# Optimization experiments

Hardware: AMD Instinct MI355X
Metric: run time of the kernel (lower is better)

The kernel has to match this reference:

```python
import jax, jax.numpy as jnp
import numpy as np

D_EMB = 1024
D_ATTN = 1024
NUM_HEADS = 16
HEAD_DIM = D_ATTN // NUM_HEADS
SEQ = 2048
BS = 2


def setup_inputs() -> dict:
    key = jax.random.key(0)
    ks = jax.random.split(key, 6)
    s = 1.0 / np.sqrt(D_EMB)
    return {
        "x": jax.random.normal(ks[0], (BS, SEQ, D_EMB), dtype=jnp.float32),
        "W_q": jax.random.uniform(ks[1], (D_ATTN, D_EMB), jnp.float32, -s, s),
        "W_k": jax.random.uniform(ks[2], (D_ATTN, D_EMB), jnp.float32, -s, s),
        "W_v": jax.random.uniform(ks[3], (D_ATTN, D_EMB), jnp.float32, -s, s),
        "W_o": jax.random.uniform(ks[4], (D_ATTN, D_ATTN), jnp.float32, -s, s),
        "b_o": jax.random.uniform(ks[5], (D_ATTN,), jnp.float32, -s, s),
    }


def reference(x, W_q, W_k, W_v, W_o, b_o):
    bs, seq_len, _ = x.shape
    # QKV projections (torch Linear: x @ W.T)
    q = jnp.einsum('bse,ae->bsa', x, W_q).reshape(bs, seq_len, NUM_HEADS, HEAD_DIM)
    k = jnp.einsum('bse,ae->bsa', x, W_k).reshape(bs, seq_len, NUM_HEADS, HEAD_DIM)
    v = jnp.einsum('bse,ae->bsa', x, W_v).reshape(bs, seq_len, NUM_HEADS, HEAD_DIM)
    # [b, h, s, d]
    q = q.transpose(0, 2, 1, 3)
    k = k.transpose(0, 2, 1, 3)
    v = v.transpose(0, 2, 1, 3)
    # scores [b, h, s, s] with causal mask
    scores = jnp.einsum('bhqd,bhkd->bhqk', q, k)
    causal = jnp.tril(jnp.ones((seq_len, seq_len), dtype=bool))
    scores = jnp.where(causal, scores, -jnp.inf)
    attn = jax.nn.softmax(scores / np.sqrt(HEAD_DIM), axis=-1)
    # dropout p=0.0 -> identity
    ctx = jnp.einsum('bhqk,bhkd->bhqd', attn, v)
    ctx = ctx.transpose(0, 2, 1, 3).reshape(bs, seq_len, D_ATTN)
    return jnp.einsum('bsa,oa->bso', ctx, W_o) + b_o
```

## Files before the change

kernel.cpp:

```cpp
#include <hip/hip_runtime.h>
#include <stdint.h>

#define SEQ   2048
#define DEMB  1024
#define NH    16
#define HD    64
#define MROWS 4096

typedef __bf16 bf16x8 __attribute__((ext_vector_type(8)));
typedef __bf16 bf16x4 __attribute__((ext_vector_type(4)));
typedef float  f32x4  __attribute__((ext_vector_type(4)));

#define MFMA(a, b, c) __builtin_amdgcn_mfma_f32_16x16x32_bf16((a), (b), (c), 0, 0, 0)

static __device__ __forceinline__ uint16_t f2bf(float f) {
  union { __bf16 b; uint16_t u; } c;
  c.b = (__bf16)f;
  return c.u;
}

static __device__ __forceinline__ ushort4 pack4(f32x4 f) {
  union { bf16x4 b; ushort4 u; } c;
  c.b[0] = (__bf16)f[0]; c.b[1] = (__bf16)f[1];
  c.b[2] = (__bf16)f[2]; c.b[3] = (__bf16)f[3];
  return c.u;
}

static __device__ __forceinline__ bf16x8 ldb8(const uint16_t* p) {
  union { uint4 i; bf16x8 b; } u;
  u.i = *(const uint4*)p;
  return u.b;
}

static __device__ __forceinline__ void gld_lds16(const uint16_t* g, uint16_t* l) {
  __builtin_amdgcn_global_load_lds(
      (const __attribute__((address_space(1))) uint32_t*)(g),
      (__attribute__((address_space(3))) uint32_t*)(l),
      16, 0, 0);
}

__global__ __launch_bounds__(256) void cvt_all(const float* __restrict__ x,
                                               const float* __restrict__ wq,
                                               const float* __restrict__ wk,
                                               const float* __restrict__ wv,
                                               const float* __restrict__ wo,
                                               uint16_t* __restrict__ xb,
                                               uint16_t* __restrict__ wqkv,
                                               uint16_t* __restrict__ wob) {
  const int bid = blockIdx.x;
  const float* src; uint16_t* dst; int off;
  if (bid < 4096)      { src = x;  dst = xb;                 off = bid; }
  else if (bid < 5120) { src = wq; dst = wqkv;               off = bid - 4096; }
  else if (bid < 6144) { src = wk; dst = wqkv + (1u << 20);  off = bid - 5120; }
  else if (bid < 7168) { src = wv; dst = wqkv + (2u << 20);  off = bid - 6144; }
  else                 { src = wo; dst = wob;                off = bid - 7168; }
  const int i = (off * 256 + threadIdx.x) * 4;
  float4 v = *(const float4*)(src + i);
  f32x4 f; f[0] = v.x; f[1] = v.y; f[2] = v.z; f[3] = v.w;
  *(ushort4*)(dst + i) = pack4(f);
}

template <int MODE>
__global__ __launch_bounds__(256) void gemm_bt(const uint16_t* __restrict__ A,
                                               const uint16_t* __restrict__ B,
                                               uint16_t* __restrict__ Cq,
                                               uint16_t* __restrict__ Ck,
                                               uint16_t* __restrict__ Cvt,
                                               float* __restrict__ Cf,
                                               const float* __restrict__ bias,
                                               int K) {
  constexpr int BN = (MODE == 2) ? 64 : 128;
  constexpr int NI = (MODE == 2) ? 2 : 4;
  __shared__ uint16_t As[2][128 * 32];
  __shared__ uint16_t Bs[2][BN * 32];
  const int t  = threadIdx.x;
  const int l  = t & 63;
  const int li = l & 15, lg = l >> 4;
  const int w  = t >> 6;
  const int wr = (w >> 1) << 6;
  const int wc = (MODE == 2) ? ((w & 1) << 5) : ((w & 1) << 6);
  const int brow = blockIdx.y << 7;
  const int bcol = blockIdx.x * BN;

  const int st_row = t >> 2;
  const int st_col = ((t & 3) ^ (st_row & 3) ^ ((st_row >> 2) & 3)) * 8;
  const uint16_t* ga0 = A + (size_t)(brow + st_row) * K + st_col;
  const uint16_t* ga1 = ga0 + (size_t)64 * K;
  const uint16_t* gb0 = B + (size_t)(bcol + st_row) * K + st_col;
  const uint16_t* gb1 = gb0 + (size_t)64 * K;

  auto stage = [&](int buf, int k0) {
    gld_lds16(ga0 + k0, &As[buf][t * 8]);
    gld_lds16(ga1 + k0, &As[buf][2048 + t * 8]);
    gld_lds16(gb0 + k0, &Bs[buf][t * 8]);
    if (BN == 128) gld_lds16(gb1 + k0, &Bs[buf][2048 + t * 8]);
  };

  const int rx = (li & 3) ^ (li >> 2);
  const int rcol = (lg ^ rx) * 8;

  f32x4 acc[4][NI] = {};

  stage(0, 0);
  __syncthreads();
  int cur = 0;

  for (int k0 = 0; k0 < K; k0 += 32) {
    if (k0 + 32 < K) stage(cur ^ 1, k0 + 32);

    bf16x8 af[4], bfr[NI];
#pragma unroll
    for (int i = 0; i < 4; ++i)
      af[i] = ldb8(&As[cur][(wr + i * 16 + li) * 32 + rcol]);
#pragma unroll
    for (int i = 0; i < NI; ++i)
      bfr[i] = ldb8(&Bs[cur][(wc + i * 16 + li) * 32 + rcol]);
#pragma unroll
    for (int mi = 0; mi < 4; ++mi)
#pragma unroll
      for (int ni = 0; ni < NI; ++ni)
        acc[mi][ni] = MFMA(af[mi], bfr[ni], acc[mi][ni]);

    __syncthreads();
    cur ^= 1;
  }

#pragma unroll
  for (int mi = 0; mi < 4; ++mi) {
#pragma unroll
    for (int ni = 0; ni < NI; ++ni) {
      const int row = brow + wr + mi * 16 + lg * 4;
      const int col = bcol + wc + ni * 16 + li;
#pragma unroll
      for (int r = 0; r < 4; ++r) {
        const float v = acc[mi][ni][r];
        if (MODE == 0) {
          if (col < 1024) {
            Cq[(size_t)(row + r) * 1024 + col] = f2bf(v * 0.18033688f);
          } else if (col < 2048) {
            Ck[(size_t)(row + r) * 1024 + (col - 1024)] = f2bf(v);
          } else {
            const int c = col - 2048;
            const int m = row + r;
            Cvt[((size_t)c + (size_t)((m >> 11) << 10)) * 2048 + (m & 2047)] = f2bf(v);
          }
        } else {
          Cf[(size_t)(row + r) * 1024 + col] = v + bias[col];
        }
      }
    }
  }
}

__global__ __launch_bounds__(256) void attn_fwd(const uint16_t* __restrict__ Q,
                                                const uint16_t* __restrict__ K,
                                                const uint16_t* __restrict__ Vt,
                                                uint16_t* __restrict__ ctx) {
  const int bh = blockIdx.x;
  const int qb = 31 - blockIdx.y;
  const int b  = bh >> 4, h = bh & 15;
  const int t  = threadIdx.x;
  const int w  = t >> 6, l = t & 63;
  const int li = l & 15, lg = l >> 4;

  __shared__ uint16_t Kl[2][64 * 64];
  __shared__ uint16_t Vl[2][64 * 64];
  __shared__ uint16_t P[4][16][72];

  const uint16_t* Kg = K + (size_t)(b * 2048) * 1024 + h * 64;
  const uint16_t* Vg = Vt + (size_t)(b * 1024 + h * 64) * 2048;

  const int srow = t >> 3;
  const int scol = ((t & 7) * 8) ^ ((srow & 7) * 8);

  const int qrow = (qb << 6) + (w << 4);
  const uint16_t* qp = Q + (size_t)(b * 2048 + qrow + li) * 1024 + h * 64 + lg * 8;
  const bf16x8 q0 = ldb8(qp);
  const bf16x8 q1 = ldb8(qp + 32);

  f32x4 o[4] = {};
  float l_r = 0.f;

  auto stage = [&](int buf, int kt2) {
    const int kb2 = kt2 << 6;
    gld_lds16(Kg + (size_t)(kb2 + srow) * 1024 + scol,      &Kl[buf][t * 8]);
    gld_lds16(Kg + (size_t)(kb2 + 32 + srow) * 1024 + scol, &Kl[buf][2048 + t * 8]);
    gld_lds16(Vg + (size_t)srow * 2048 + kb2 + scol,        &Vl[buf][t * 8]);
    gld_lds16(Vg + (size_t)(32 + srow) * 2048 + kb2 + scol, &Vl[buf][2048 + t * 8]);
  };

  stage(0, 0);
  __syncthreads();
  int cur = 0;

  const int fsw = (li & 7) * 8;

  for (int kt = 0; kt <= qb; ++kt) {
    if (kt < qb) stage(cur ^ 1, kt + 1);

    const uint16_t* Kc = &Kl[cur][0];
    const uint16_t* Vc = &Vl[cur][0];

    f32x4 s[4];
    __builtin_amdgcn_s_setprio(1);
#pragma unroll
    for (int tt = 0; tt < 4; ++tt) {
      const uint16_t* kr = Kc + (tt * 16 + li) * 64;
      f32x4 z = {};
      z = MFMA(ldb8(kr + ((lg * 8) ^ fsw)), q0, z);
      z = MFMA(ldb8(kr + ((32 + lg * 8) ^ fsw)), q1, z);
      s[tt] = z;
    }
    __builtin_amdgcn_s_setprio(0);

    bf16x8 vf[4][2];
#pragma unroll
    for (int dt = 0; dt < 4; ++dt) {
      const uint16_t* vr = Vc + (dt * 16 + li) * 64;
      vf[dt][0] = ldb8(vr + ((lg * 8) ^ fsw));
      vf[dt][1] = ldb8(vr + ((32 + lg * 8) ^ fsw));
    }

    if (kt == qb) {
      const int qloc = (w << 4) + li;
#pragma unroll
      for (int tt = 0; tt < 4; ++tt) {
        const int key = (tt << 4) + (lg << 2);
#pragma unroll
        for (int r = 0; r < 4; ++r)
          if (key + r > qloc) s[tt][r] = -1e30f;
      }
    }

    float lsum = 0.f;
    ushort4 pk[4];
#pragma unroll
    for (int tt = 0; tt < 4; ++tt) {
      f32x4 p;
      p[0] = __builtin_amdgcn_exp2f(s[tt][0]);
      p[1] = __builtin_amdgcn_exp2f(s[tt][1]);
      p[2] = __builtin_amdgcn_exp2f(s[tt][2]);
      p[3] = __builtin_amdgcn_exp2f(s[tt][3]);
      lsum += (p[0] + p[1]) + (p[2] + p[3]);
      pk[tt] = pack4(p);
    }
    l_r += lsum;

#pragma unroll
    for (int tt = 0; tt < 4; ++tt)
      *(ushort4*)&P[w][li][(tt << 4) + (lg << 2)] = pk[tt];
    asm volatile("s_waitcnt lgkmcnt(0)" ::: "memory");

    const bf16x8 pb0 = ldb8(&P[w][li][lg * 8]);
    const bf16x8 pb1 = ldb8(&P[w][li][32 + lg * 8]);
    __builtin_amdgcn_s_setprio(1);
#pragma unroll
    for (int dt = 0; dt < 4; ++dt) {
      o[dt] = MFMA(vf[dt][0], pb0, o[dt]);
      o[dt] = MFMA(vf[dt][1], pb1, o[dt]);
    }
    __builtin_amdgcn_s_setprio(0);

    __syncthreads();
    cur ^= 1;
  }

  l_r += __shfl_xor(l_r, 16);
  l_r += __shfl_xor(l_r, 32);
  const float inv = 1.0f / l_r;
  const int qg = b * 2048 + qrow + li;
#pragma unroll
  for (int dt = 0; dt < 4; ++dt) {
    f32x4 ov = o[dt];
    ov[0] *= inv; ov[1] *= inv; ov[2] *= inv; ov[3] *= inv;
    *(ushort4*)(ctx + (size_t)qg * 1024 + h * 64 + (dt << 4) + (lg << 2)) = pack4(ov);
  }
}

extern "C" void kernel_launch(void* const* d_in, const int* in_sizes, int n_in,
                              void* d_out, int out_size, void* d_ws, size_t ws_size,
                              hipStream_t stream) {
  const float* x  = (const float*)d_in[0];
  const float* Wq = (const float*)d_in[1];
  const float* Wk = (const float*)d_in[2];
  const float* Wv = (const float*)d_in[3];
  const float* Wo = (const float*)d_in[4];
  const float* bo = (const float*)d_in[5];
  float* out = (float*)d_out;

  char* ws = (char*)d_ws;
  uint16_t* xb   = (uint16_t*)(ws);
  uint16_t* Wqkv = (uint16_t*)(ws + ( 8u << 20));
  uint16_t* Wob  = (uint16_t*)(ws + (14u << 20));
  uint16_t* Qb   = (uint16_t*)(ws + (16u << 20));
  uint16_t* Kb   = (uint16_t*)(ws + (24u << 20));
  uint16_t* Vt   = (uint16_t*)(ws + (32u << 20));
  uint16_t* Ctx  = (uint16_t*)(ws);

  cvt_all<<<8192, 256, 0, stream>>>(x, Wq, Wk, Wv, Wo, xb, Wqkv, Wob);

  gemm_bt<0><<<dim3(24, 32), 256, 0, stream>>>(xb, Wqkv, Qb, Kb, Vt,
                                               nullptr, nullptr, 1024);

  attn_fwd<<<dim3(32, 32), 256, 0, stream>>>(Qb, Kb, Vt, Ctx);

  gemm_bt<2><<<dim3(16, 32), 256, 0, stream>>>(Ctx, Wob, nullptr, nullptr, nullptr,
                                               out, bo, 1024);
}
```

Measured before the change: 112.1 us.

## Use 512-thread blocks, K=64 stages, XCD-aware block swizzle for GEMMs and attention

Both GEMMs move to 512-thread blocks with eight waves, a 64-wide K stage with an XOR swizzle for LDS, and a 1D grid remapped so each group of eight consecutive block IDs covers a contiguous chunk of tiles. The aim is better L2 locality per XCD and fewer barriers per K. Attention now handles 128 query rows per block with eight waves sharing each K/V tile, and orders (batch, head) pairs by XCD. This halves K/V staging per query, though each wave now waits on more barriers and causal masking spans two diagonal tiles.

```diff
diff --git a/kernel.cpp b/kernel.cpp
--- a/kernel.cpp
+++ b/kernel.cpp
@@ -61,43 +61,55 @@
 }
 
 template <int MODE>
-__global__ __launch_bounds__(256) void gemm_bt(const uint16_t* __restrict__ A,
+__global__ __launch_bounds__(512) void gemm_bt(const uint16_t* __restrict__ A,
                                                const uint16_t* __restrict__ B,
                                                uint16_t* __restrict__ Cq,
                                                uint16_t* __restrict__ Ck,
                                                uint16_t* __restrict__ Cvt,
                                                float* __restrict__ Cf,
-                                               const float* __restrict__ bias,
-                                               int K) {
-  constexpr int BN = (MODE == 2) ? 64 : 128;
-  constexpr int NI = (MODE == 2) ? 2 : 4;
-  __shared__ uint16_t As[2][128 * 32];
-  __shared__ uint16_t Bs[2][BN * 32];
+                                               const float* __restrict__ bias) {
+  constexpr int K   = 1024;
+  constexpr int BN  = (MODE == 0) ? 128 : 64;
+  constexpr int NI  = (MODE == 0) ? 2 : 1;
+  constexpr int NBX = (MODE == 0) ? 24 : 16;
+  constexpr int CHUNK = (MODE == 0) ? 96 : 64;
+
+  __shared__ uint16_t As[2][128 * 64];
+  __shared__ uint16_t Bs[2][BN * 64];
+
+  const int id  = blockIdx.x;
+  const int swz = (id & 7) * CHUNK + (id >> 3);
+  const int brow = (swz / NBX) << 7;
+  const int bcol = (swz % NBX) * BN;
+
   const int t  = threadIdx.x;
   const int l  = t & 63;
   const int li = l & 15, lg = l >> 4;
   const int w  = t >> 6;
-  const int wr = (w >> 1) << 6;
-  const int wc = (MODE == 2) ? ((w & 1) << 5) : ((w & 1) << 6);
-  const int brow = blockIdx.y << 7;
-  const int bcol = blockIdx.x * BN;
-
-  const int st_row = t >> 2;
-  const int st_col = ((t & 3) ^ (st_row & 3) ^ ((st_row >> 2) & 3)) * 8;
-  const uint16_t* ga0 = A + (size_t)(brow + st_row) * K + st_col;
-  const uint16_t* ga1 = ga0 + (size_t)64 * K;
-  const uint16_t* gb0 = B + (size_t)(bcol + st_row) * K + st_col;
-  const uint16_t* gb1 = gb0 + (size_t)64 * K;
+  const int wm = w >> 2;
+  const int wn = w & 3;
+
+  const int srow = t >> 3;
+  const int scol = ((t & 7) ^ (srow & 7)) << 3;
+  const uint16_t* gA = A + (size_t)(brow + srow) * K + scol;
+  const uint16_t* gB = B + (size_t)(bcol + srow) * K + scol;
 
   auto stage = [&](int buf, int k0) {
-    gld_lds16(ga0 + k0, &As[buf][t * 8]);
-    gld_lds16(ga1 + k0, &As[buf][2048 + t * 8]);
-    gld_lds16(gb0 + k0, &Bs[buf][t * 8]);
-    if (BN == 128) gld_lds16(gb1 + k0, &Bs[buf][2048 + t * 8]);
+    gld_lds16(gA + k0, &As[buf][t * 8]);
+    gld_lds16(gA + (size_t)64 * K + k0, &As[buf][4096 + t * 8]);
+    gld_lds16(gB + k0, &Bs[buf][t * 8]);
+    if (MODE == 0) gld_lds16(gB + (size_t)64 * K + k0, &Bs[buf][4096 + t * 8]);
   };
 
-  const int rx = (li & 3) ^ (li >> 2);
-  const int rcol = (lg ^ rx) * 8;
+  const int sw = li & 7;
+  auto ldA = [&](int buf, int kh, int fi) {
+    const int row = wm * 64 + fi * 16 + li;
+    return ldb8(&As[buf][(row << 6) + ((((kh << 2) + lg) ^ sw) << 3)]);
+  };
+  auto ldB = [&](int buf, int kh, int ni) {
+    const int row = wn * (BN / 4) + ni * 16 + li;
+    return ldb8(&Bs[buf][(row << 6) + ((((kh << 2) + lg) ^ sw) << 3)]);
+  };
 
   f32x4 acc[4][NI] = {};
 
@@ -105,21 +117,24 @@
   __syncthreads();
   int cur = 0;
 
-  for (int k0 = 0; k0 < K; k0 += 32) {
-    if (k0 + 32 < K) stage(cur ^ 1, k0 + 32);
-
-    bf16x8 af[4], bfr[NI];
-#pragma unroll
-    for (int i = 0; i < 4; ++i)
-      af[i] = ldb8(&As[cur][(wr + i * 16 + li) * 32 + rcol]);
-#pragma unroll
-    for (int i = 0; i < NI; ++i)
-      bfr[i] = ldb8(&Bs[cur][(wc + i * 16 + li) * 32 + rcol]);
-#pragma unroll
-    for (int mi = 0; mi < 4; ++mi)
-#pragma unroll
-      for (int ni = 0; ni < NI; ++ni)
-        acc[mi][ni] = MFMA(af[mi], bfr[ni], acc[mi][ni]);
+  for (int k0 = 0; k0 < K; k0 += 64) {
+    if (k0 + 64 < K) stage(cur ^ 1, k0 + 64);
+
+#pragma unroll
+    for (int kh = 0; kh < 2; ++kh) {
+      bf16x8 af[4], bfr[NI];
+#pragma unroll
+      for (int fi = 0; fi < 4; ++fi) af[fi] = ldA(cur, kh, fi);
+#pragma unroll
+      for (int ni = 0; ni < NI; ++ni) bfr[ni] = ldB(cur, kh, ni);
+      __builtin_amdgcn_s_setprio(1);
+#pragma unroll
+      for (int fi = 0; fi < 4; ++fi)
+#pragma unroll
+        for (int ni = 0; ni < NI; ++ni)
+          acc[fi][ni] = MFMA(af[fi], bfr[ni], acc[fi][ni]);
+      __builtin_amdgcn_s_setprio(0);
+    }
 
     __syncthreads();
     cur ^= 1;
@@ -129,8 +144,8 @@
   for (int mi = 0; mi < 4; ++mi) {
 #pragma unroll
     for (int ni = 0; ni < NI; ++ni) {
-      const int row = brow + wr + mi * 16 + lg * 4;
-      const int col = bcol + wc + ni * 16 + li;
+      const int row = brow + wm * 64 + mi * 16 + lg * 4;
+      const int col = bcol + wn * (BN / 4) + ni * 16 + li;
 #pragma unroll
       for (int r = 0; r < 4; ++r) {
         const float v = acc[mi][ni][r];
@@ -152,20 +167,23 @@
   }
 }
 
-__global__ __launch_bounds__(256) void attn_fwd(const uint16_t* __restrict__ Q,
+__global__ __launch_bounds__(512) void attn_fwd(const uint16_t* __restrict__ Q,
                                                 const uint16_t* __restrict__ K,
                                                 const uint16_t* __restrict__ Vt,
                                                 uint16_t* __restrict__ ctx) {
-  const int bh = blockIdx.x;
-  const int qb = 31 - blockIdx.y;
-  const int b  = bh >> 4, h = bh & 15;
+  const int id   = blockIdx.x;
+  const int rank = id >> 3;
+  const int bh   = (id & 7) * 4 + (rank >> 4);
+  const int qbl  = 15 - (rank & 15);
+  const int b = bh >> 4, h = bh & 15;
+
   const int t  = threadIdx.x;
   const int w  = t >> 6, l = t & 63;
   const int li = l & 15, lg = l >> 4;
 
   __shared__ uint16_t Kl[2][64 * 64];
   __shared__ uint16_t Vl[2][64 * 64];
-  __shared__ uint16_t P[4][16][72];
+  __shared__ uint16_t P[8][16][72];
 
   const uint16_t* Kg = K + (size_t)(b * 2048) * 1024 + h * 64;
   const uint16_t* Vg = Vt + (size_t)(b * 1024 + h * 64) * 2048;
@@ -173,7 +191,7 @@
   const int srow = t >> 3;
   const int scol = ((t & 7) * 8) ^ ((srow & 7) * 8);
 
-  const int qrow = (qb << 6) + (w << 4);
+  const int qrow = (qbl << 7) + (w << 4);
   const uint16_t* qp = Q + (size_t)(b * 2048 + qrow + li) * 1024 + h * 64 + lg * 8;
   const bf16x8 q0 = ldb8(qp);
   const bf16x8 q1 = ldb8(qp + 32);
@@ -183,10 +201,8 @@
 
   auto stage = [&](int buf, int kt2) {
     const int kb2 = kt2 << 6;
-    gld_lds16(Kg + (size_t)(kb2 + srow) * 1024 + scol,      &Kl[buf][t * 8]);
-    gld_lds16(Kg + (size_t)(kb2 + 32 + srow) * 1024 + scol, &Kl[buf][2048 + t * 8]);
-    gld_lds16(Vg + (size_t)srow * 2048 + kb2 + scol,        &Vl[buf][t * 8]);
-    gld_lds16(Vg + (size_t)(32 + srow) * 2048 + kb2 + scol, &Vl[buf][2048 + t * 8]);
+    gld_lds16(Kg + (size_t)(kb2 + srow) * 1024 + scol, &Kl[buf][t * 8]);
+    gld_lds16(Vg + (size_t)srow * 2048 + kb2 + scol,   &Vl[buf][t * 8]);
   };
 
   stage(0, 0);
@@ -194,9 +210,11 @@
   int cur = 0;
 
   const int fsw = (li & 7) * 8;
-
-  for (int kt = 0; kt <= qb; ++kt) {
-    if (kt < qb) stage(cur ^ 1, kt + 1);
+  const int nkt = (qbl << 1) + 2;
+  const int qglob = qrow + li;
+
+  for (int kt = 0; kt < nkt; ++kt) {
+    if (kt < nkt - 1) stage(cur ^ 1, kt + 1);
 
     const uint16_t* Kc = &Kl[cur][0];
     const uint16_t* Vc = &Vl[cur][0];
@@ -221,14 +239,14 @@
       vf[dt][1] = ldb8(vr + ((32 + lg * 8) ^ fsw));
     }
 
-    if (kt == qb) {
-      const int qloc = (w << 4) + li;
+    if ((kt << 6) + 63 > qrow) {
+      const int kb = kt << 6;
 #pragma unroll
       for (int tt = 0; tt < 4; ++tt) {
-        const int key = (tt << 4) + (lg << 2);
+        const int key = kb + (tt << 4) + (lg << 2);
 #pragma unroll
         for (int r = 0; r < 4; ++r)
-          if (key + r > qloc) s[tt][r] = -1e30f;
+          if (key + r > qglob) s[tt][r] = -1e30f;
       }
     }
 
@@ -299,11 +317,9 @@
 
   cvt_all<<<8192, 256, 0, stream>>>(x, Wq, Wk, Wv, Wo, xb, Wqkv, Wob);
 
-  gemm_bt<0><<<dim3(24, 32), 256, 0, stream>>>(xb, Wqkv, Qb, Kb, Vt,
-                                               nullptr, nullptr, 1024);
-
-  attn_fwd<<<dim3(32, 32), 256, 0, stream>>>(Qb, Kb, Vt, Ctx);
-
-  gemm_bt<2><<<dim3(16, 32), 256, 0, stream>>>(Ctx, Wob, nullptr, nullptr, nullptr,
-                                               out, bo, 1024);
-}
+  gemm_bt<0><<<768, 512, 0, stream>>>(xb, Wqkv, Qb, Kb, Vt, nullptr, nullptr);
+
+  attn_fwd<<<512, 512, 0, stream>>>(Qb, Kb, Vt, Ctx);
+
+  gemm_bt<2><<<512, 512, 0, stream>>>(Ctx, Wob, nullptr, nullptr, nullptr, out, bo);
+}
```

Result: slower. 122.8 us (+9.6%).
